# Kernel optimization log

Hardware: AMD Instinct MI355X
Metric: run time of the kernel (lower is better)

Reference implementation:

```python
import jax, jax.numpy as jnp
import numpy as np

TINY = 1e-13  # tiny_value_of_dtype(float32)


def gru_cell(x, h, Wx, Wh, bx, bh):
    gx = x @ Wx + bx
    gh = h @ Wh + bh
    xr, xz, xn = jnp.split(gx, 3, -1)
    hr, hz, hn = jnp.split(gh, 3, -1)
    r = jax.nn.sigmoid(xr + hr)
    z = jax.nn.sigmoid(xz + hz)
    n = jnp.tanh(xn + r * hn)
    return (1.0 - z) * n + z * h


def setup_inputs() -> dict:
    B, V, VT, D, OPT, SEQ, SRC = 256, 2000, 10000, 256, 16, 10, 40
    key = jax.random.key(0)
    ks = jax.random.split(key, 20)
    rn = lambda i, shape, s: jax.random.normal(ks[i], shape, jnp.float32) * s
    inp = {}
    inp['lhs'] = jax.random.randint(ks[0], (B,), 0, V)
    inp['lhs_mask'] = jnp.ones((B,), jnp.int32)
    inp['tree_state'] = rn(1, (B, D), 1.0)
    sym = jax.random.randint(ks[2], (B, OPT, SEQ), 0, V)
    pg = jax.random.randint(ks[3], (B, OPT, SEQ), 0, 2)
    fg = jax.random.randint(ks[4], (B, OPT, SEQ), 0, 2)
    lens = jax.random.randint(ks[5], (B, OPT), 1, SEQ + 1)
    msk = (jnp.arange(SEQ)[None, None, :] < lens[:, :, None]).astype(jnp.int32)
    inp['grammar_guide'] = jnp.stack([sym, pg, fg, msk], axis=2)  # (B,OPT,4,SEQ)
    inp['emb'] = rn(6, (V, D), 0.02)
    inp['mem'] = rn(7, (B, SRC, D), 1.0)  # encoder memory for query_attn_fn
    inp['Wx'] = rn(8, (D, 3 * D), 0.05)
    inp['Wh'] = rn(9, (D, 3 * D), 0.05)
    inp['bx'] = jnp.zeros((3 * D,), jnp.float32)
    inp['bh'] = jnp.zeros((3 * D,), jnp.float32)
    inp['Wc'] = rn(10, (2 * D, D), 0.05)
    inp['bc'] = jnp.zeros((D,), jnp.float32)
    inp['Wsym'] = rn(11, (D, V), 0.05)
    inp['bsym'] = jnp.zeros((V,), jnp.float32)
    inp['Wtok'] = rn(12, (2 * D, VT), 0.05)
    inp['btok'] = jnp.zeros((VT,), jnp.float32)
    inp['tok_table'] = (jax.random.uniform(ks[13], (V, VT)) < 0.05).astype(jnp.float32)
    return inp


def reference(lhs, lhs_mask, tree_state, grammar_guide, emb, mem, Wx, Wh, bx, bh,
              Wc, bc, Wsym, bsym, Wtok, btok, tok_table):
    B, OPT, _, SEQ = grammar_guide.shape
    V = emb.shape[0]
    D = emb.shape[1]
    g_sym = grammar_guide[:, :, 0, :]   # (B,OPT,SEQ) symbol options
    g_mask = grammar_guide[:, :, 3, :]  # (B,OPT,SEQ) option mask

    def step_fn(carry, xs):
        step_inp, ts = carry
        opts, omask = xs  # (B,OPT) ints
        x = emb[step_inp]                      # embedding (dropout = identity, eval mode)
        # hx re-initialized each step from the fixed pre-step tree state
        h = gru_cell(x, tree_state, Wx, Wh, bx, bh)  # (B,D) step_out
        att = jax.nn.softmax(jnp.einsum('bd,bsd->bs', h, mem), axis=-1)
        ctx = jnp.einsum('bs,bsd->bd', att, mem)
        step_out_att = jnp.tanh(jnp.concatenate([ctx, h], -1) @ Wc + bc)
        logits = step_out_att @ Wsym + bsym    # (B,V)
        ts_new = jnp.tanh(ts + step_out_att)   # tree state updater
        # grammar compliance masking
        comp = opts * omask                    # (B,OPT)
        w = jnp.sum(jax.nn.one_hot(comp, V, dtype=jnp.float32), axis=1) > 0  # (B,V) bool
        w0 = jnp.sum((comp == 0) * omask, axis=-1) > 0
        w = w.at[:, 0].set(w0)
        clogits = logits + jnp.log(w.astype(logits.dtype) + TINY)
        nxt = jnp.argmax(clogits, axis=-1)     # free-running next input
        return (nxt, ts_new), clogits

    xs = (jnp.moveaxis(g_sym, -1, 0), jnp.moveaxis(g_mask, -1, 0))  # (SEQ,B,OPT)
    (_, ts_final), seq_logits = jax.lax.scan(step_fn, (lhs, tree_state), xs)
    seq_logits = jnp.moveaxis(seq_logits, 0, -1)                 # (B,V,SEQ)
    seq_logp = jnp.log(jax.nn.softmax(seq_logits, axis=1) + TINY)
    seq_opts_logp = jnp.take_along_axis(seq_logp, g_sym, axis=1)  # (B,OPT,SEQ)
    opts_logp = jnp.sum(seq_opts_logp * g_mask, axis=-1)          # (B,OPT)

    # tree topology inference: pick best option row of grammar_guide
    best = jnp.argmax(opts_logp, axis=-1)
    topo = jnp.take_along_axis(grammar_guide, best[:, None, None, None], axis=1)[:, 0]  # (B,4,SEQ)
    symbol, p_growth, f_growth, mask = topo[:, 0], topo[:, 1], topo[:, 2], topo[:, 3]

    # exact token prediction after derivation
    cw = tok_table[symbol]                     # (B,SEQ,VT) token compliance
    s_emb = emb[symbol]                        # (B,SEQ,D)
    ts_tiled = jnp.broadcast_to(ts_final[:, None, :], (B, SEQ, D))
    proj = jnp.concatenate([s_emb, ts_tiled], axis=-1)
    exact_logit = proj @ Wtok + btok + jnp.log(cw + TINY)  # (B,SEQ,VT)

    return (lhs, lhs_mask, grammar_guide, opts_logp,
            (symbol, p_growth, f_growth, mask), exact_logit)
```

## Files before the change

kernel.cpp:

```cpp
#include <hip/hip_runtime.h>
#include <math.h>

#define BB 256
#define DD 256
#define VV 2000
#define VT 10000
#define OPTN 16
#define SEQN 10
#define SRCN 40
#define D3 768
#define D2 512

#define LOG_TINY (-29.9336062f)

#define OFF_OPTS  (2*BB + BB*OPTN*4*SEQN)
#define OFF_TOPO  (OFF_OPTS + BB*OPTN)
#define OFF_EXACT (OFF_TOPO + 4*BB*SEQN)

#define TOKB_STRIDE 320
#define TOKB_W 313

#define NWG_TOK 1580

typedef __bf16 bf16x8 __attribute__((ext_vector_type(8)));
typedef float  f32x4  __attribute__((ext_vector_type(4)));

__device__ __forceinline__ float sigm(float x){ return 1.0f/(1.0f+expf(-x)); }
__device__ __forceinline__ unsigned short f2bf(float x){
  union { float f; unsigned int u; } v; v.f = x;
  unsigned int r = (v.u + 0x7FFF + ((v.u >> 16) & 1)) >> 16;
  return (unsigned short)r;
}

__global__ void k_gh(const float* __restrict__ ts0, const float* __restrict__ Wh,
                     const float* __restrict__ bh, float* __restrict__ gh){
  int b = blockIdx.x;
  int j = blockIdx.y*256 + threadIdx.x;
  __shared__ float hsh[DD];
  hsh[threadIdx.x] = ts0[b*DD + threadIdx.x];
  __syncthreads();
  float a0 = bh[j], a1 = 0.f, a2 = 0.f, a3 = 0.f;
  #pragma unroll 4
  for(int k=0;k<DD;k+=4){
    a0 = fmaf(hsh[k+0], Wh[(k+0)*D3 + j], a0);
    a1 = fmaf(hsh[k+1], Wh[(k+1)*D3 + j], a1);
    a2 = fmaf(hsh[k+2], Wh[(k+2)*D3 + j], a2);
    a3 = fmaf(hsh[k+3], Wh[(k+3)*D3 + j], a3);
  }
  gh[b*D3 + j] = (a0+a1)+(a2+a3);
}

__global__ void k_ew(const float* __restrict__ emb, const float* __restrict__ Wx,
                     float* __restrict__ EW){
  __shared__ float As[16][64];
  __shared__ float Bs[16][64];
  int tid = threadIdx.x;
  int tx = tid & 15, ty = tid >> 4;
  int m0 = blockIdx.y*64, n0 = blockIdx.x*64;
  float acc[4][4];
  #pragma unroll
  for(int i=0;i<4;i++){ acc[i][0]=0.f; acc[i][1]=0.f; acc[i][2]=0.f; acc[i][3]=0.f; }
  for(int k0=0;k0<DD;k0+=16){
    {
      int row = tid >> 2, kk = (tid & 3)*4;
      int m = m0 + row;
      float4 av = {0,0,0,0};
      if(m < VV) av = *(const float4*)&emb[m*DD + k0 + kk];
      As[kk+0][row]=av.x; As[kk+1][row]=av.y; As[kk+2][row]=av.z; As[kk+3][row]=av.w;
    }
    {
      int r = tid >> 4, c2 = (tid & 15)*4;
      float4 bv = *(const float4*)&Wx[(k0+r)*D3 + n0 + c2];
      *(float4*)&Bs[r][c2] = bv;
    }
    __syncthreads();
    #pragma unroll
    for(int k=0;k<16;k++){
      float4 a4 = *(const float4*)&As[k][ty*4];
      float4 b4 = *(const float4*)&Bs[k][tx*4];
      float av[4] = {a4.x,a4.y,a4.z,a4.w};
      float bw[4] = {b4.x,b4.y,b4.z,b4.w};
      #pragma unroll
      for(int i=0;i<4;i++)
        #pragma unroll
        for(int j=0;j<4;j++) acc[i][j] = fmaf(av[i], bw[j], acc[i][j]);
    }
    __syncthreads();
  }
  #pragma unroll
  for(int i=0;i<4;i++){
    int m = m0 + ty*4 + i;
    if(m < VV){
      #pragma unroll
      for(int j=0;j<4;j++) EW[m*D3 + n0 + tx*4 + j] = acc[i][j];
    }
  }
}

__global__ void k_wtokT(const float* __restrict__ Wtok, unsigned short* __restrict__ WtokB){
  __shared__ float tile[32][65];
  int tid = threadIdx.x;
  int n0 = blockIdx.x*64, k0 = blockIdx.y*32;
  #pragma unroll
  for(int p=0;p<8;p++){
    int idx = tid + p*256;
    int kk = idx >> 6, nn = idx & 63;
    int n = n0 + nn;
    tile[kk][nn] = (n < VT) ? Wtok[(size_t)(k0+kk)*VT + n] : 0.f;
  }
  __syncthreads();
  #pragma unroll
  for(int p=0;p<4;p++){
    int idx = tid + p*256;
    int nn = idx >> 4, kk = (idx & 15)*2;
    int n = n0 + nn;
    if(n < VT){
      ushort2 v;
      v.x = f2bf(tile[kk][nn]);
      v.y = f2bf(tile[kk+1][nn]);
      *(ushort2*)&WtokB[(size_t)n*D2 + k0 + kk] = v;
    }
  }
}

__global__ __launch_bounds__(256) void k_tokbits(const float* __restrict__ tok_table,
                                                 unsigned int* __restrict__ bits){
  int idx = blockIdx.x*256 + threadIdx.x;
  const int total = VV*TOKB_W;
  for(; idx < total; idx += gridDim.x*256){
    int v = idx / TOKB_W, w = idx - v*TOKB_W;
    const float* row = tok_table + (size_t)v*VT + w*32;
    unsigned int bv = 0;
    if(w*32 + 32 <= VT){
      #pragma unroll
      for(int k=0;k<8;k++){
        float4 x = *(const float4*)(row + k*4);
        bv |= (x.x>0.5f?1u:0u) << (k*4+0);
        bv |= (x.y>0.5f?1u:0u) << (k*4+1);
        bv |= (x.z>0.5f?1u:0u) << (k*4+2);
        bv |= (x.w>0.5f?1u:0u) << (k*4+3);
      }
    } else {
      for(int k=0;k<32;k++){
        int n = w*32 + k;
        if(n < VT && row[k] > 0.5f) bv |= 1u << k;
      }
    }
    bits[v*TOKB_STRIDE + w] = bv;
  }
}

__global__ __launch_bounds__(512) void k_chain(
    const int* __restrict__ lhs, const float* __restrict__ EW,
    const float* __restrict__ gh, const float* __restrict__ bx,
    const float* __restrict__ tree_state, const float* __restrict__ mem,
    const float* __restrict__ Wc, const float* __restrict__ bc,
    const float* __restrict__ Wsym, const float* __restrict__ bsym,
    const int* __restrict__ gg, float* __restrict__ soa_all,
    float* __restrict__ ts){
  int b = blockIdx.x, tid = threadIdx.x;
  int lane = tid & 63, wv = tid >> 6;
  __shared__ float memsh[SRCN][DD];
  __shared__ float bxsh[D3];
  __shared__ float ghsh[D3];
  __shared__ float bcsh[DD];
  __shared__ float tssh[DD];
  __shared__ float hsh[DD], csh[DD], soash[DD];
  __shared__ float psum[2][DD];
  __shared__ float sc[SRCN];
  __shared__ int cvs[16];
  __shared__ float cvals[16];
  __shared__ int symsh;
  __shared__ float wmax[8]; __shared__ int widx[8];

  for(int i = tid; i < SRCN*DD; i += 512) ((float*)memsh)[i] = mem[(size_t)b*SRCN*DD + i];
  for(int i = tid; i < D3; i += 512){ bxsh[i] = bx[i]; ghsh[i] = gh[(size_t)b*D3 + i]; }
  if(tid < DD){ bcsh[tid] = bc[tid]; tssh[tid] = tree_state[b*DD + tid]; }
  float t0 = (tid < DD) ? tree_state[b*DD + tid] : 0.f;
  if(tid == 0) symsh = lhs[b];
  __syncthreads();

  for(int t = 0; t < SEQN; t++){
    int sym = symsh;
    if(tid < 16){
      int base = ((b*OPTN + tid)*4)*SEQN + t;
      int mk = gg[base + 3*SEQN];
      cvs[tid] = mk ? gg[base] : -1;
    }
    if(tid < DD){
      const float* ew = EW + (size_t)sym*D3;
      float r = sigm(ew[tid]     + bxsh[tid]     + ghsh[tid]);
      float z = sigm(ew[256+tid] + bxsh[256+tid] + ghsh[256+tid]);
      float n = tanhf(ew[512+tid] + bxsh[512+tid] + r*ghsh[512+tid]);
      hsh[tid] = (1.0f - z)*n + z*t0;
    }
    __syncthreads();
    for(int s = wv; s < SRCN; s += 8){
      float p = 0.f;
      #pragma unroll 4
      for(int d = lane; d < DD; d += 64) p = fmaf(hsh[d], memsh[s][d], p);
      for(int off=32; off; off>>=1) p += __shfl_down(p, off, 64);
      if(lane == 0) sc[s] = p;
    }
    __syncthreads();
    if(tid < 64){
      float v = (tid < SRCN) ? sc[tid] : -1e30f;
      float mx = v;
      for(int off=32; off; off>>=1) mx = fmaxf(mx, __shfl_xor(mx, off, 64));
      float e = (tid < SRCN) ? expf(v - mx) : 0.f;
      float su = e;
      for(int off=32; off; off>>=1) su += __shfl_xor(su, off, 64);
      if(tid < SRCN) sc[tid] = e / su;
    }
    __syncthreads();
    if(tid < DD){
      float c = 0.f;
      #pragma unroll 8
      for(int s=0;s<SRCN;s++) c = fmaf(sc[s], memsh[s][tid], c);
      csh[tid] = c;
    }
    __syncthreads();
    {
      int j = tid & 255, half = tid >> 8;
      const float* src = half ? hsh : csh;
      const float* w = Wc + (size_t)half*256*DD + j;
      float a0=0.f, a1=0.f, a2=0.f, a3=0.f;
      #pragma unroll 4
      for(int k=0;k<256;k+=4){
        a0 = fmaf(src[k+0], w[(size_t)(k+0)*DD], a0);
        a1 = fmaf(src[k+1], w[(size_t)(k+1)*DD], a1);
        a2 = fmaf(src[k+2], w[(size_t)(k+2)*DD], a2);
        a3 = fmaf(src[k+3], w[(size_t)(k+3)*DD], a3);
      }
      psum[half][j] = (a0+a1)+(a2+a3);
    }
    __syncthreads();
    if(tid < DD){
      float sv = tanhf(psum[0][tid] + psum[1][tid] + bcsh[tid]);
      soash[tid] = sv;
      soa_all[(size_t)(t*BB + b)*DD + tid] = sv;
      tssh[tid] = tanhf(tssh[tid] + sv);
    }
    __syncthreads();
    bool anyc = false;
    #pragma unroll
    for(int i=0;i<16;i++) anyc |= (cvs[i] >= 0);
    if(anyc){
      if(tid < 256){
        int g = tid >> 4, l = tid & 15;
        int v = cvs[g];
        float d = 0.f;
        if(v >= 0){
          #pragma unroll
          for(int k=0;k<16;k++) d = fmaf(soash[l*16+k], Wsym[(size_t)(l*16+k)*VV + v], d);
        }
        d += __shfl_xor(d, 1, 64); d += __shfl_xor(d, 2, 64);
        d += __shfl_xor(d, 4, 64); d += __shfl_xor(d, 8, 64);
        if(l == 0) cvals[g] = (v >= 0) ? d + bsym[v] : -3.0e30f;
      }
      __syncthreads();
      if(tid == 0){
        float bvv = -3.0e30f; int bnn = 0x7FFFFFFF;
        #pragma unroll
        for(int g=0; g<16; g++){
          int v = cvs[g];
          if(v >= 0){
            float val = cvals[g];
            if(val > bvv || (val == bvv && v < bnn)){ bvv = val; bnn = v; }
          }
        }
        symsh = bnn;
      }
      __syncthreads();
    } else {
      float bv = -3.0e30f; int bn = 0x7FFFFFFF;
      if(tid < 500){
        int c0 = tid*4;
        const float* wcol = Wsym + c0;
        float4 a = {0.f,0.f,0.f,0.f};
        #pragma unroll 8
        for(int k=0;k<DD;k++){
          float sk = soash[k];
          float4 w4 = *(const float4*)(wcol + (size_t)k*VV);
          a.x = fmaf(sk, w4.x, a.x);
          a.y = fmaf(sk, w4.y, a.y);
          a.z = fmaf(sk, w4.z, a.z);
          a.w = fmaf(sk, w4.w, a.w);
        }
        #pragma unroll
        for(int j=0;j<4;j++){
          int n = c0 + j;
          float val = ((float*)&a)[j] + bsym[n] + LOG_TINY;
          if(val > bv){ bv = val; bn = n; }
        }
      }
      #pragma unroll
      for(int off=1; off<64; off<<=1){
        float ov = __shfl_xor(bv, off, 64);
        int   on = __shfl_xor(bn, off, 64);
        if(ov > bv || (ov == bv && on < bn)){ bv = ov; bn = on; }
      }
      if(lane == 0){ wmax[wv] = bv; widx[wv] = bn; }
      __syncthreads();
      if(tid == 0){
        float m = wmax[0]; int mi = widx[0];
        #pragma unroll
        for(int w=1; w<8; w++)
          if(wmax[w] > m || (wmax[w] == m && widx[w] < mi)){ m = wmax[w]; mi = widx[w]; }
        symsh = mi;
      }
      __syncthreads();
    }
  }
  if(tid < DD) ts[b*DD + tid] = tssh[tid];
}

__global__ void k_cl(const float* __restrict__ A, const float* __restrict__ Wsym,
                     const float* __restrict__ bsym, const int* __restrict__ gg,
                     float* __restrict__ cl){
  __shared__ float As[16][32];
  __shared__ float Bs[16][64];
  __shared__ unsigned int selb[32][2];
  int tid = threadIdx.x;
  int tx = tid & 15, ty = tid >> 4;
  int m0 = blockIdx.y*32, n0 = blockIdx.x*64;
  if(tid < 64) selb[tid>>1][tid&1] = 0u;
  __syncthreads();
  for(int idx = tid; idx < 32*OPTN; idx += 256){
    int i = idx >> 4, o = idx & 15;
    int m = m0 + i;
    int bb = m & (BB-1), t = m >> 8;
    int base = ((bb*OPTN + o)*4)*SEQN + t;
    int mk = gg[base + 3*SEQN];
    int v = mk ? gg[base] : -1;
    unsigned int d = (unsigned int)(v - n0);
    if(d < 64u) atomicOr(&selb[i][d>>5], 1u << (d&31));
  }
  float acc[2][4];
  #pragma unroll
  for(int i=0;i<2;i++){ acc[i][0]=0.f; acc[i][1]=0.f; acc[i][2]=0.f; acc[i][3]=0.f; }
  for(int k0=0;k0<DD;k0+=16){
    if(tid < 128){
      int row = tid >> 2, kk = (tid & 3)*4;
      float4 av = *(const float4*)&A[(size_t)(m0+row)*DD + k0 + kk];
      As[kk+0][row]=av.x; As[kk+1][row]=av.y; As[kk+2][row]=av.z; As[kk+3][row]=av.w;
    }
    {
      int r = tid >> 4, c2 = (tid & 15)*4;
      int n = n0 + c2;
      float4 bv;
      if(n + 3 < VV){ bv = *(const float4*)&Wsym[(k0+r)*VV + n]; }
      else {
        bv.x = (n+0<VV)? Wsym[(k0+r)*VV + n+0] : 0.f;
        bv.y = (n+1<VV)? Wsym[(k0+r)*VV + n+1] : 0.f;
        bv.z = (n+2<VV)? Wsym[(k0+r)*VV + n+2] : 0.f;
        bv.w = (n+3<VV)? Wsym[(k0+r)*VV + n+3] : 0.f;
      }
      *(float4*)&Bs[r][c2] = bv;
    }
    __syncthreads();
    #pragma unroll
    for(int k=0;k<16;k++){
      float a0 = As[k][ty*2+0];
      float a1 = As[k][ty*2+1];
      float4 b4 = *(const float4*)&Bs[k][tx*4];
      acc[0][0] = fmaf(a0, b4.x, acc[0][0]);
      acc[0][1] = fmaf(a0, b4.y, acc[0][1]);
      acc[0][2] = fmaf(a0, b4.z, acc[0][2]);
      acc[0][3] = fmaf(a0, b4.w, acc[0][3]);
      acc[1][0] = fmaf(a1, b4.x, acc[1][0]);
      acc[1][1] = fmaf(a1, b4.y, acc[1][1]);
      acc[1][2] = fmaf(a1, b4.z, acc[1][2]);
      acc[1][3] = fmaf(a1, b4.w, acc[1][3]);
    }
    __syncthreads();
  }
  #pragma unroll
  for(int i=0;i<2;i++){
    int m = m0 + ty*2 + i;
    unsigned int s0 = selb[ty*2+i][0], s1 = selb[ty*2+i][1];
    float vals[4];
    #pragma unroll
    for(int j=0;j<4;j++){
      int n = n0 + tx*4 + j;
      int nn = tx*4 + j;
      unsigned int wb = (nn < 32) ? s0 : s1;
      vals[j] = acc[i][j] + ((n < VV) ? bsym[n] : 0.f) + (((wb >> (nn&31)) & 1u) ? 0.f : LOG_TINY);
    }
    int nb = n0 + tx*4;
    if(nb + 3 < VV){
      float4 o; o.x=vals[0]; o.y=vals[1]; o.z=vals[2]; o.w=vals[3];
      *(float4*)&cl[(size_t)m*VV + nb] = o;
    } else {
      #pragma unroll
      for(int j=0;j<4;j++){
        int n = nb + j;
        if(n < VV) cl[(size_t)m*VV + n] = vals[j];
      }
    }
  }
}

__global__ void k_lse(const float* __restrict__ cl, float* __restrict__ lse_g){
  int m = blockIdx.x;
  int tid = threadIdx.x, lane = tid & 63, wv = tid >> 6;
  __shared__ float redm[4], reds[4];
  const float* row = cl + (size_t)m*VV;
  float mx = -1e30f;
  for(int v=tid; v<VV; v+=256) mx = fmaxf(mx, row[v]);
  for(int off=32; off; off>>=1) mx = fmaxf(mx, __shfl_xor(mx, off, 64));
  if(lane==0) redm[wv] = mx;
  __syncthreads();
  float gmx = fmaxf(fmaxf(redm[0],redm[1]), fmaxf(redm[2],redm[3]));
  float sum = 0.f;
  for(int v=tid; v<VV; v+=256) sum += expf(row[v]-gmx);
  for(int off=32; off; off>>=1) sum += __shfl_xor(sum, off, 64);
  if(lane==0) reds[wv] = sum;
  __syncthreads();
  if(tid==0) lse_g[m] = gmx + logf(reds[0]+reds[1]+reds[2]+reds[3]);
}

__global__ void k_opts(const float* __restrict__ cl, const float* __restrict__ lse_g,
                       const int* __restrict__ gg, const float* __restrict__ emb,
                       const float* __restrict__ ts, float* __restrict__ out,
                       int* __restrict__ sym_i, unsigned short* __restrict__ A){
  int b = blockIdx.x, tid = threadIdx.x;
  __shared__ float lse_sh[SEQN];
  __shared__ float sacc[OPTN];
  __shared__ int ssym[SEQN];
  __shared__ int sbest;
  if(tid < SEQN) lse_sh[tid] = lse_g[tid*BB + b];
  __syncthreads();
  if(tid < OPTN){
    int o = tid;
    float acc = 0.f;
    for(int t=0;t<SEQN;t++){
      int base = ((b*OPTN + o)*4)*SEQN + t;
      int mk = gg[base + 3*SEQN];
      if(mk){
        int v = gg[base];
        float p = expf(cl[((size_t)t*BB + b)*VV + v] - lse_sh[t]);
        acc += logf(p + 1e-13f);
      }
    }
    sacc[o] = acc;
    out[OFF_OPTS + b*OPTN + o] = acc;
  }
  __syncthreads();
  if(tid==0){
    float mx = sacc[0]; int mi = 0;
    for(int o=1;o<OPTN;o++) if(sacc[o] > mx){ mx = sacc[o]; mi = o; }
    sbest = mi;
  }
  __syncthreads();
  if(tid < 4*SEQN){
    int c = tid/SEQN, t = tid%SEQN;
    int val = gg[((b*OPTN + sbest)*4 + c)*SEQN + t];
    out[OFF_TOPO + c*(BB*SEQN) + b*SEQN + t] = (float)val;
    if(c==0){ sym_i[b*SEQN + t] = val; ssym[t] = val; }
  }
  __syncthreads();
  for(int idx = tid; idx < SEQN*D2; idx += 256){
    int t = idx >> 9, k = idx & 511;
    float val = (k < DD) ? emb[ssym[t]*DD + k] : ts[b*DD + (k-DD)];
    A[(size_t)(b*SEQN + t)*D2 + k] = f2bf(val);
  }
}

__global__ void k_pass(const int* __restrict__ lhs, const int* __restrict__ lhs_mask,
                       const int* __restrict__ gg, float* __restrict__ out){
  int i = blockIdx.x*256 + threadIdx.x;
  if(i < BB) out[i] = (float)lhs[i];
  else if(i < 2*BB) out[i] = (float)lhs_mask[i - BB];
  else if(i < 2*BB + BB*OPTN*4*SEQN) out[2*BB + (i - 2*BB)] = (float)gg[i - 2*BB];
}

__global__ __launch_bounds__(256) void k_tok_mfma(
    const unsigned short* __restrict__ A, const unsigned short* __restrict__ Bw,
    const float* __restrict__ btok, const unsigned int* __restrict__ tokbits,
    const int* __restrict__ sym_i, float* __restrict__ out){
  __shared__ __align__(16) unsigned short Ssh[4*5120];
  __shared__ float sBtok[128];
  int tid = threadIdx.x;
  int lane = tid & 63, wave = tid >> 6;
  int c = lane & 15, q = lane >> 4;
  int wm = (wave >> 1)*64, wn = (wave & 1)*64;

  int id = blockIdx.x;
  int xcd = id & 7, off = id >> 3;
  const int qq = NWG_TOK >> 3, rr = NWG_TOK & 7;
  int start = (xcd < rr) ? xcd*(qq+1) : rr*(qq+1) + (xcd-rr)*qq;
  int ord = start + off;
  int mb = ord % 20, nb = ord / 20;
  int m0 = mb*128, n0 = nb*128;

  if(tid < 128){
    int n = n0 + tid;
    sBtok[tid] = (n < VT) ? btok[n] : 0.f;
  }
  f32x4 acc[4][4];
  #pragma unroll
  for(int i=0;i<4;i++)
    #pragma unroll
    for(int j=0;j<4;j++) acc[i][j] = (f32x4){0.f,0.f,0.f,0.f};

  int arow = tid >> 2;
  int ach  = (tid & 3) * 8;
  const size_t aoff0 = (size_t)(m0 + arow)*D2 + ach;
  const size_t aoff1 = (size_t)(m0 + 64 + arow)*D2 + ach;
  int bn0 = n0 + arow, bn1 = n0 + 64 + arow;
  bool b0ok = bn0 < VT, b1ok = bn1 < VT;
  const size_t boff0 = (size_t)bn0*D2 + ach;
  const size_t boff1 = (size_t)bn1*D2 + ach;
  const float4 f0 = {0.f,0.f,0.f,0.f};

  float4 ra0 = *(const float4*)(A + aoff0);
  float4 ra1 = *(const float4*)(A + aoff1);
  float4 rb0 = b0ok ? *(const float4*)(Bw + boff0) : f0;
  float4 rb1 = b1ok ? *(const float4*)(Bw + boff1) : f0;

  for(int t=0; t<16; t++){
    unsigned short* As = Ssh + (t&1)*10240;
    unsigned short* Bs = As + 5120;
    *(float4*)(As + arow*40 + ach)      = ra0;
    *(float4*)(As + (64+arow)*40 + ach) = ra1;
    *(float4*)(Bs + arow*40 + ach)      = rb0;
    *(float4*)(Bs + (64+arow)*40 + ach) = rb1;
    __syncthreads();
    if(t < 15){
      int k0 = (t+1)*32;
      ra0 = *(const float4*)(A + aoff0 + k0);
      ra1 = *(const float4*)(A + aoff1 + k0);
      if(b0ok) rb0 = *(const float4*)(Bw + boff0 + k0);
      if(b1ok) rb1 = *(const float4*)(Bw + boff1 + k0);
    }
    bf16x8 af[4], bf[4];
    #pragma unroll
    for(int i=0;i<4;i++) af[i] = *(const bf16x8*)(As + (wm + i*16 + c)*40 + q*8);
    #pragma unroll
    for(int j=0;j<4;j++) bf[j] = *(const bf16x8*)(Bs + (wn + j*16 + c)*40 + q*8);
    #pragma unroll
    for(int i=0;i<4;i++)
      #pragma unroll
      for(int j=0;j<4;j++)
        acc[i][j] = __builtin_amdgcn_mfma_f32_16x16x32_bf16(af[i], bf[j], acc[i][j], 0, 0, 0);
  }
  __syncthreads();

  float* sw = (float*)Ssh + wave*(64*21);
  int lrow = lane >> 2, ln4 = lane & 3;
  #pragma unroll
  for(int i=0;i<4;i++){
    #pragma unroll
    for(int j=0;j<4;j++){
      int col = j*16 + c;
      #pragma unroll
      for(int r2=0;r2<4;r2++) sw[col*21 + q*4 + r2] = acc[i][j][r2];
    }
    int row_g = m0 + wm + i*16 + lrow;
    int s = sym_i[row_g];
    const unsigned int* bt = tokbits + (size_t)s*TOKB_STRIDE;
    float* orow = out + OFF_EXACT + (size_t)row_g*VT;
    #pragma unroll
    for(int s4=0;s4<4;s4++){
      int colo = ln4*4 + s4*16;
      int n = n0 + wn + colo;
      if(n < VT){
        float4 bt4 = *(const float4*)&sBtok[wn + colo];
        unsigned int wb = bt[n >> 5];
        int sh = n & 31;
        float4 o;
        o.x = sw[(colo+0)*21 + lrow] + bt4.x + (((wb>>(sh+0))&1u) ? 0.f : LOG_TINY);
        o.y = sw[(colo+1)*21 + lrow] + bt4.y + (((wb>>(sh+1))&1u) ? 0.f : LOG_TINY);
        o.z = sw[(colo+2)*21 + lrow] + bt4.z + (((wb>>(sh+2))&1u) ? 0.f : LOG_TINY);
        o.w = sw[(colo+3)*21 + lrow] + bt4.w + (((wb>>(sh+3))&1u) ? 0.f : LOG_TINY);
        *(float4*)(orow + n) = o;
      }
    }
  }
}

extern "C" void kernel_launch(void* const* d_in, const int* in_sizes, int n_in,
                              void* d_out, int out_size, void* d_ws, size_t ws_size,
                              hipStream_t stream) {
  const int*   lhs       = (const int*)  d_in[0];
  const int*   lhs_mask  = (const int*)  d_in[1];
  const float* tree_state= (const float*)d_in[2];
  const int*   gg        = (const int*)  d_in[3];
  const float* emb       = (const float*)d_in[4];
  const float* mem       = (const float*)d_in[5];
  const float* Wx        = (const float*)d_in[6];
  const float* Wh        = (const float*)d_in[7];
  const float* bx        = (const float*)d_in[8];
  const float* bh        = (const float*)d_in[9];
  const float* Wc        = (const float*)d_in[10];
  const float* bc        = (const float*)d_in[11];
  const float* Wsym      = (const float*)d_in[12];
  const float* bsym      = (const float*)d_in[13];
  const float* Wtok      = (const float*)d_in[14];
  const float* btok      = (const float*)d_in[15];
  const float* tok_table = (const float*)d_in[16];
  float* out = (float*)d_out;

  float* W       = (float*)d_ws;
  float* gh      = W;
  float* ts      = gh + BB*D3;
  float* soa_all = ts + BB*DD;
  float* cl      = soa_all + (size_t)SEQN*BB*DD;
  float* EW      = cl + (size_t)SEQN*BB*VV;
  float* lse_g   = EW + VV*D3;
  int*   sym_i   = (int*)(lse_g + SEQN*BB);
  unsigned short* Abf  = (unsigned short*)(sym_i + BB*SEQN);
  unsigned short* WtokB= Abf + (size_t)BB*SEQN*D2;
  unsigned int* tokbits= (unsigned int*)(WtokB + (size_t)VT*D2);

  k_pass<<<(2*BB + BB*OPTN*4*SEQN + 255)/256, 256, 0, stream>>>(lhs, lhs_mask, gg, out);
  k_tokbits<<<2048, 256, 0, stream>>>(tok_table, tokbits);
  k_wtokT<<<dim3((VT+63)/64, D2/32), 256, 0, stream>>>(Wtok, WtokB);
  k_gh<<<dim3(BB,3), 256, 0, stream>>>(tree_state, Wh, bh, gh);
  k_ew<<<dim3(D3/64, (VV+63)/64), 256, 0, stream>>>(emb, Wx, EW);

  k_chain<<<BB, 512, 0, stream>>>(lhs, EW, gh, bx, tree_state, mem, Wc, bc,
                                  Wsym, bsym, gg, soa_all, ts);

  k_cl<<<dim3(32, 80), 256, 0, stream>>>(soa_all, Wsym, bsym, gg, cl);
  k_lse<<<SEQN*BB, 256, 0, stream>>>(cl, lse_g);
  k_opts<<<BB, 256, 0, stream>>>(cl, lse_g, gg, emb, ts, out, sym_i, Abf);
  k_tok_mfma<<<NWG_TOK, 256, 0, stream>>>(Abf, WtokB, btok, tokbits, sym_i, out);
}
```

Baseline: 569.9 us.

## Process two batch rows per workgroup in the sequential chain kernel

The chain kernel now handles two batch elements per 512-thread workgroup instead of one. Each Wc weight load is reused for both rows, and all threads are busy in the GRU, context and store phases. The mem tile is no longer staged in shared memory and is read straight from global memory. The trade-off is half as many workgroups (128) on a GPU with many CUs, and the full-vocabulary argmax fallback now runs serially per row.

```diff
diff --git a/kernel.cpp b/kernel.cpp
--- a/kernel.cpp
+++ b/kernel.cpp
@@ -158,161 +158,196 @@
     const float* __restrict__ Wsym, const float* __restrict__ bsym,
     const int* __restrict__ gg, float* __restrict__ soa_all,
     float* __restrict__ ts){
-  int b = blockIdx.x, tid = threadIdx.x;
+  int tid = threadIdx.x;
   int lane = tid & 63, wv = tid >> 6;
-  __shared__ float memsh[SRCN][DD];
-  __shared__ float bxsh[D3];
-  __shared__ float ghsh[D3];
-  __shared__ float bcsh[DD];
-  __shared__ float tssh[DD];
-  __shared__ float hsh[DD], csh[DD], soash[DD];
-  __shared__ float psum[2][DD];
-  __shared__ float sc[SRCN];
-  __shared__ int cvs[16];
-  __shared__ float cvals[16];
-  __shared__ int symsh;
+  int b0 = blockIdx.x * 2;
+  __shared__ float bxsh[D3], bcsh[DD];
+  __shared__ float ghsh[2][D3];
+  __shared__ float t0sh[2][DD], tssh[2][DD];
+  __shared__ float hsh[2][DD], csh[2][DD], soash[2][DD];
+  __shared__ float psum[2][2][DD];
+  __shared__ float sc[2][SRCN];
+  __shared__ int   cvs[2][16];
+  __shared__ float cvals[2][16];
+  __shared__ int   symsh[2];
+  __shared__ int   eflag[2];
   __shared__ float wmax[8]; __shared__ int widx[8];
 
-  for(int i = tid; i < SRCN*DD; i += 512) ((float*)memsh)[i] = mem[(size_t)b*SRCN*DD + i];
-  for(int i = tid; i < D3; i += 512){ bxsh[i] = bx[i]; ghsh[i] = gh[(size_t)b*D3 + i]; }
-  if(tid < DD){ bcsh[tid] = bc[tid]; tssh[tid] = tree_state[b*DD + tid]; }
-  float t0 = (tid < DD) ? tree_state[b*DD + tid] : 0.f;
-  if(tid == 0) symsh = lhs[b];
+  for(int i = tid; i < D3; i += 512){
+    bxsh[i] = bx[i];
+    ghsh[0][i] = gh[(size_t)b0*D3 + i];
+    ghsh[1][i] = gh[(size_t)(b0+1)*D3 + i];
+  }
+  {
+    int bb = tid >> 8, j = tid & 255;
+    float tv = tree_state[(b0+bb)*DD + j];
+    t0sh[bb][j] = tv; tssh[bb][j] = tv;
+    if(tid < DD) bcsh[tid] = bc[tid];
+    if(tid < 2) symsh[tid] = lhs[b0+tid];
+  }
   __syncthreads();
 
   for(int t = 0; t < SEQN; t++){
-    int sym = symsh;
-    if(tid < 16){
-      int base = ((b*OPTN + tid)*4)*SEQN + t;
+    if(tid < 32){
+      int bb = tid >> 4, o = tid & 15;
+      int base = (((b0+bb)*OPTN + o)*4)*SEQN + t;
       int mk = gg[base + 3*SEQN];
-      cvs[tid] = mk ? gg[base] : -1;
-    }
-    if(tid < DD){
+      cvs[bb][o] = mk ? gg[base] : -1;
+    }
+    {
+      int bb = tid >> 8, j = tid & 255;
+      int sym = symsh[bb];
       const float* ew = EW + (size_t)sym*D3;
-      float r = sigm(ew[tid]     + bxsh[tid]     + ghsh[tid]);
-      float z = sigm(ew[256+tid] + bxsh[256+tid] + ghsh[256+tid]);
-      float n = tanhf(ew[512+tid] + bxsh[512+tid] + r*ghsh[512+tid]);
-      hsh[tid] = (1.0f - z)*n + z*t0;
-    }
-    __syncthreads();
-    for(int s = wv; s < SRCN; s += 8){
-      float p = 0.f;
-      #pragma unroll 4
-      for(int d = lane; d < DD; d += 64) p = fmaf(hsh[d], memsh[s][d], p);
-      for(int off=32; off; off>>=1) p += __shfl_down(p, off, 64);
-      if(lane == 0) sc[s] = p;
-    }
-    __syncthreads();
-    if(tid < 64){
-      float v = (tid < SRCN) ? sc[tid] : -1e30f;
+      float r = sigm(ew[j]     + bxsh[j]     + ghsh[bb][j]);
+      float z = sigm(ew[256+j] + bxsh[256+j] + ghsh[bb][256+j]);
+      float n = tanhf(ew[512+j] + bxsh[512+j] + r*ghsh[bb][512+j]);
+      hsh[bb][j] = (1.0f - z)*n + z*t0sh[bb][j];
+    }
+    __syncthreads();
+    {
+      int bb = wv >> 2, w4 = wv & 3;
+      const float* hb = hsh[bb];
+      #pragma unroll 2
+      for(int s = w4; s < SRCN; s += 4){
+        const float* mrow = mem + (size_t)((b0+bb)*SRCN + s)*DD;
+        float p = 0.f;
+        #pragma unroll 4
+        for(int d = lane; d < DD; d += 64) p = fmaf(hb[d], mrow[d], p);
+        for(int off=32; off; off>>=1) p += __shfl_down(p, off, 64);
+        if(lane == 0) sc[bb][s] = p;
+      }
+    }
+    __syncthreads();
+    if(wv < 2){
+      float v = (lane < SRCN) ? sc[wv][lane] : -1e30f;
       float mx = v;
       for(int off=32; off; off>>=1) mx = fmaxf(mx, __shfl_xor(mx, off, 64));
-      float e = (tid < SRCN) ? expf(v - mx) : 0.f;
+      float e = (lane < SRCN) ? expf(v - mx) : 0.f;
       float su = e;
       for(int off=32; off; off>>=1) su += __shfl_xor(su, off, 64);
-      if(tid < SRCN) sc[tid] = e / su;
-    }
-    __syncthreads();
-    if(tid < DD){
+      if(lane < SRCN) sc[wv][lane] = e / su;
+    }
+    __syncthreads();
+    {
+      int bb = tid >> 8, d = tid & 255;
+      const float* mb = mem + (size_t)(b0+bb)*SRCN*DD + d;
       float c = 0.f;
       #pragma unroll 8
-      for(int s=0;s<SRCN;s++) c = fmaf(sc[s], memsh[s][tid], c);
-      csh[tid] = c;
+      for(int s=0;s<SRCN;s++) c = fmaf(sc[bb][s], mb[(size_t)s*DD], c);
+      csh[bb][d] = c;
     }
     __syncthreads();
     {
       int j = tid & 255, half = tid >> 8;
-      const float* src = half ? hsh : csh;
       const float* w = Wc + (size_t)half*256*DD + j;
-      float a0=0.f, a1=0.f, a2=0.f, a3=0.f;
+      const float* s0 = half ? hsh[0] : csh[0];
+      const float* s1 = half ? hsh[1] : csh[1];
+      float a00=0.f,a01=0.f,a02=0.f,a03=0.f;
+      float a10=0.f,a11=0.f,a12=0.f,a13=0.f;
       #pragma unroll 4
       for(int k=0;k<256;k+=4){
-        a0 = fmaf(src[k+0], w[(size_t)(k+0)*DD], a0);
-        a1 = fmaf(src[k+1], w[(size_t)(k+1)*DD], a1);
-        a2 = fmaf(src[k+2], w[(size_t)(k+2)*DD], a2);
-        a3 = fmaf(src[k+3], w[(size_t)(k+3)*DD], a3);
-      }
-      psum[half][j] = (a0+a1)+(a2+a3);
-    }
-    __syncthreads();
-    if(tid < DD){
-      float sv = tanhf(psum[0][tid] + psum[1][tid] + bcsh[tid]);
-      soash[tid] = sv;
-      soa_all[(size_t)(t*BB + b)*DD + tid] = sv;
-      tssh[tid] = tanhf(tssh[tid] + sv);
-    }
-    __syncthreads();
-    bool anyc = false;
-    #pragma unroll
-    for(int i=0;i<16;i++) anyc |= (cvs[i] >= 0);
-    if(anyc){
-      if(tid < 256){
-        int g = tid >> 4, l = tid & 15;
-        int v = cvs[g];
-        float d = 0.f;
+        float w0 = w[(size_t)(k+0)*DD];
+        float w1 = w[(size_t)(k+1)*DD];
+        float w2 = w[(size_t)(k+2)*DD];
+        float w3 = w[(size_t)(k+3)*DD];
+        a00 = fmaf(s0[k+0], w0, a00); a01 = fmaf(s0[k+1], w1, a01);
+        a02 = fmaf(s0[k+2], w2, a02); a03 = fmaf(s0[k+3], w3, a03);
+        a10 = fmaf(s1[k+0], w0, a10); a11 = fmaf(s1[k+1], w1, a11);
+        a12 = fmaf(s1[k+2], w2, a12); a13 = fmaf(s1[k+3], w3, a13);
+      }
+      psum[0][half][j] = (a00+a01)+(a02+a03);
+      psum[1][half][j] = (a10+a11)+(a12+a13);
+    }
+    __syncthreads();
+    {
+      int bb = tid >> 8, j = tid & 255;
+      float sv = tanhf(psum[bb][0][j] + psum[bb][1][j] + bcsh[j]);
+      soash[bb][j] = sv;
+      soa_all[(size_t)(t*BB + b0+bb)*DD + j] = sv;
+      tssh[bb][j] = tanhf(tssh[bb][j] + sv);
+    }
+    if(tid < 2){
+      bool any = false;
+      #pragma unroll
+      for(int i=0;i<16;i++) any |= (cvs[tid][i] >= 0);
+      eflag[tid] = any ? 1 : 0;
+    }
+    __syncthreads();
+    {
+      int grp = tid >> 4, l = tid & 15;
+      int bb = grp >> 4, g = grp & 15;
+      int v = cvs[bb][g];
+      float d = 0.f;
+      if(v >= 0){
+        const float* sb = soash[bb];
+        #pragma unroll
+        for(int k=0;k<16;k++) d = fmaf(sb[l*16+k], Wsym[(size_t)(l*16+k)*VV + v], d);
+      }
+      d += __shfl_xor(d, 1, 64); d += __shfl_xor(d, 2, 64);
+      d += __shfl_xor(d, 4, 64); d += __shfl_xor(d, 8, 64);
+      if(l == 0) cvals[bb][g] = (v >= 0) ? d + bsym[v] : -3.0e30f;
+    }
+    __syncthreads();
+    if(tid < 2 && eflag[tid]){
+      float bvv = -3.0e30f; int bnn = 0x7FFFFFFF;
+      #pragma unroll
+      for(int g=0; g<16; g++){
+        int v = cvs[tid][g];
         if(v >= 0){
+          float val = cvals[tid][g];
+          if(val > bvv || (val == bvv && v < bnn)){ bvv = val; bnn = v; }
+        }
+      }
+      symsh[tid] = bnn;
+    }
+    __syncthreads();
+    for(int bb = 0; bb < 2; bb++){
+      if(!eflag[bb]){
+        float bv = -3.0e30f; int bn = 0x7FFFFFFF;
+        if(tid < 500){
+          int c0 = tid*4;
+          const float* wcol = Wsym + c0;
+          const float* sb = soash[bb];
+          float4 a = {0.f,0.f,0.f,0.f};
+          #pragma unroll 8
+          for(int k=0;k<DD;k++){
+            float sk = sb[k];
+            float4 w4 = *(const float4*)(wcol + (size_t)k*VV);
+            a.x = fmaf(sk, w4.x, a.x);
+            a.y = fmaf(sk, w4.y, a.y);
+            a.z = fmaf(sk, w4.z, a.z);
+            a.w = fmaf(sk, w4.w, a.w);
+          }
           #pragma unroll
-          for(int k=0;k<16;k++) d = fmaf(soash[l*16+k], Wsym[(size_t)(l*16+k)*VV + v], d);
-        }
-        d += __shfl_xor(d, 1, 64); d += __shfl_xor(d, 2, 64);
-        d += __shfl_xor(d, 4, 64); d += __shfl_xor(d, 8, 64);
-        if(l == 0) cvals[g] = (v >= 0) ? d + bsym[v] : -3.0e30f;
-      }
-      __syncthreads();
-      if(tid == 0){
-        float bvv = -3.0e30f; int bnn = 0x7FFFFFFF;
-        #pragma unroll
-        for(int g=0; g<16; g++){
-          int v = cvs[g];
-          if(v >= 0){
-            float val = cvals[g];
-            if(val > bvv || (val == bvv && v < bnn)){ bvv = val; bnn = v; }
+          for(int j=0;j<4;j++){
+            int n = c0 + j;
+            float val = ((float*)&a)[j] + bsym[n] + LOG_TINY;
+            if(val > bv){ bv = val; bn = n; }
           }
         }
-        symsh = bnn;
-      }
-      __syncthreads();
-    } else {
-      float bv = -3.0e30f; int bn = 0x7FFFFFFF;
-      if(tid < 500){
-        int c0 = tid*4;
-        const float* wcol = Wsym + c0;
-        float4 a = {0.f,0.f,0.f,0.f};
-        #pragma unroll 8
-        for(int k=0;k<DD;k++){
-          float sk = soash[k];
-          float4 w4 = *(const float4*)(wcol + (size_t)k*VV);
-          a.x = fmaf(sk, w4.x, a.x);
-          a.y = fmaf(sk, w4.y, a.y);
-          a.z = fmaf(sk, w4.z, a.z);
-          a.w = fmaf(sk, w4.w, a.w);
+        #pragma unroll
+        for(int off=1; off<64; off<<=1){
+          float ov = __shfl_xor(bv, off, 64);
+          int   on = __shfl_xor(bn, off, 64);
+          if(ov > bv || (ov == bv && on < bn)){ bv = ov; bn = on; }
         }
-        #pragma unroll
-        for(int j=0;j<4;j++){
-          int n = c0 + j;
-          float val = ((float*)&a)[j] + bsym[n] + LOG_TINY;
-          if(val > bv){ bv = val; bn = n; }
+        if(lane == 0){ wmax[wv] = bv; widx[wv] = bn; }
+        __syncthreads();
+        if(tid == 0){
+          float m = wmax[0]; int mi = widx[0];
+          #pragma unroll
+          for(int w=1; w<8; w++)
+            if(wmax[w] > m || (wmax[w] == m && widx[w] < mi)){ m = wmax[w]; mi = widx[w]; }
+          symsh[bb] = mi;
         }
-      }
-      #pragma unroll
-      for(int off=1; off<64; off<<=1){
-        float ov = __shfl_xor(bv, off, 64);
-        int   on = __shfl_xor(bn, off, 64);
-        if(ov > bv || (ov == bv && on < bn)){ bv = ov; bn = on; }
-      }
-      if(lane == 0){ wmax[wv] = bv; widx[wv] = bn; }
-      __syncthreads();
-      if(tid == 0){
-        float m = wmax[0]; int mi = widx[0];
-        #pragma unroll
-        for(int w=1; w<8; w++)
-          if(wmax[w] > m || (wmax[w] == m && widx[w] < mi)){ m = wmax[w]; mi = widx[w]; }
-        symsh = mi;
-      }
-      __syncthreads();
-    }
-  }
-  if(tid < DD) ts[b*DD + tid] = tssh[tid];
+        __syncthreads();
+      }
+    }
+  }
+  {
+    int bb = tid >> 8, j = tid & 255;
+    ts[(b0+bb)*DD + j] = tssh[bb][j];
+  }
 }
 
 __global__ void k_cl(const float* __restrict__ A, const float* __restrict__ Wsym,
@@ -620,8 +655,8 @@
   k_gh<<<dim3(BB,3), 256, 0, stream>>>(tree_state, Wh, bh, gh);
   k_ew<<<dim3(D3/64, (VV+63)/64), 256, 0, stream>>>(emb, Wx, EW);
 
-  k_chain<<<BB, 512, 0, stream>>>(lhs, EW, gh, bx, tree_state, mem, Wc, bc,
-                                  Wsym, bsym, gg, soa_all, ts);
+  k_chain<<<BB/2, 512, 0, stream>>>(lhs, EW, gh, bx, tree_state, mem, Wc, bc,
+                                    Wsym, bsym, gg, soa_all, ts);
 
   k_cl<<<dim3(32, 80), 256, 0, stream>>>(soa_all, Wsym, bsym, gg, cl);
   k_lse<<<SEQN*BB, 256, 0, stream>>>(cl, lse_g);
```

Result: slower. 630.8 us (+10.7%).
